# Performance work log

Hardware: AMD Instinct MI355X
Metric: run time of the kernel (lower is better)

## Reference

```python
import jax, jax.numpy as jnp
import numpy as np

N = 100000      # num nodes
E = 262144      # num directed edges (symmetrized)
DIN, H1, H2 = 58, 300, 100
EPS = 1e-15


def _glorot(k, shape):
    lim = float(np.sqrt(6.0 / (shape[0] + shape[1])))
    return jax.random.uniform(k, shape, jnp.float32, -lim, lim)


def setup_inputs() -> dict:
    key = jax.random.key(0)
    ks = jax.random.split(key, 16)
    x = jax.random.normal(ks[0], (N, DIN), jnp.float32)
    half = jax.random.randint(ks[1], (2, E // 2), 0, N, dtype=jnp.int32)
    edge_index = jnp.concatenate([half, half[::-1]], axis=1)  # symmetric graph
    neg_edge_index = jax.random.randint(ks[2], (2, E), 0, N, dtype=jnp.int32)
    return {
        "x": x,
        "edge_index": edge_index,
        "neg_edge_index": neg_edge_index,
        "conv1_w0": _glorot(ks[3], (DIN, H1)),
        "conv1_w1": _glorot(ks[4], (DIN, H1)),
        "conv1_b": jnp.zeros((H1,), jnp.float32),
        "conv2_w0": _glorot(ks[5], (H1, H2)),
        "conv2_w1": _glorot(ks[6], (H1, H2)),
        "conv2_b": jnp.zeros((H2,), jnp.float32),
        "conv3_w0": _glorot(ks[7], (H2, 1)),
        "conv3_w1": _glorot(ks[8], (H2, 1)),
        "conv3_b": jnp.zeros((1,), jnp.float32),
        "lin1_w": _glorot(ks[9], (DIN, H2)),
        "lin1_b": jnp.zeros((H2,), jnp.float32),
        "lin2_w": _glorot(ks[10], (DIN, H2)),
        "lin2_b": jnp.zeros((H2,), jnp.float32),
        "c1": jnp.array([0.5], jnp.float32),
        "c2": jnp.array([0.5], jnp.float32),
    }


def _cheb_norm(edge_index, n):
    # ChebConv K=2, sym normalization, lambda_max=2: edge weight = -d^-1/2 * d^-1/2
    row, col = edge_index[0], edge_index[1]
    deg = jax.ops.segment_sum(jnp.ones((edge_index.shape[1],), jnp.float32), row,
                              num_segments=n)
    dinv = jnp.where(deg > 0, jax.lax.rsqrt(jnp.maximum(deg, 1.0)), 0.0)
    return -dinv[row] * dinv[col]


def _cheb_conv(x, edge_index, w, w0, w1, b):
    # out = Tx0 @ W0 + Tx1 @ W1 + b, with Tx1 = -(D^-1/2 A D^-1/2) x
    src, dst = edge_index[0], edge_index[1]
    tx1 = jax.ops.segment_sum(w[:, None] * x[src], dst, num_segments=x.shape[0])
    return x @ w0 + tx1 @ w1 + b


def _link_logits(z, ei):
    return jnp.sum(z[ei[0]] * z[ei[1]], axis=1)


def reference(x, edge_index, neg_edge_index,
              conv1_w0, conv1_w1, conv1_b,
              conv2_w0, conv2_w1, conv2_b,
              conv3_w0, conv3_w1, conv3_b,
              lin1_w, lin1_b, lin2_w, lin2_b, c1, c2):
    n = x.shape[0]
    w = _cheb_norm(edge_index, n)  # eval mode: dropout_edge is identity
    x0 = x                          # eval mode: F.dropout is identity
    h = jax.nn.relu(_cheb_conv(x0, edge_index, w, conv1_w0, conv1_w1, conv1_b))
    x1 = jax.nn.relu(_cheb_conv(h, edge_index, w, conv2_w0, conv2_w1, conv2_b))
    xs = x1 + jax.nn.relu(x0 @ lin1_w + lin1_b)
    z = x1 + jax.nn.relu(x0 @ lin2_w + lin2_b)
    pos_loss = -jnp.mean(jnp.log(jax.nn.sigmoid(_link_logits(z, edge_index)) + EPS))
    neg_loss = -jnp.mean(jnp.log(1.0 - jax.nn.sigmoid(_link_logits(z, neg_edge_index)) + EPS))
    r_loss = pos_loss + neg_loss
    out = _cheb_conv(xs, edge_index, w, conv3_w0, conv3_w1, conv3_b).squeeze(-1)
    return (out, r_loss, c1, c2)
```

## Files before the change

### kernel.cpp

```cpp
#include <hip/hip_runtime.h>
#include <hip/hip_bf16.h>
#include <cstddef>

#define DIN 58
#define H1  300
#define H2  100

using bf16x8 = __attribute__((ext_vector_type(8))) short;
using bf16x4 = __attribute__((ext_vector_type(4))) short;
using f32x4  = __attribute__((ext_vector_type(4))) float;

__device__ inline unsigned short f2bf(float f) {
    union { float f; unsigned int u; } v; v.f = f;
    unsigned int r = v.u + 0x7fff + ((v.u >> 16) & 1);
    return (unsigned short)(r >> 16);
}
__device__ inline float bf2f(unsigned short h) {
    union { unsigned int u; float f; } v; v.u = ((unsigned int)h) << 16;
    return v.f;
}


__global__ void k_zero(float* __restrict__ p, long n) {
    long i = (long)blockIdx.x * 256 + threadIdx.x;
    long stride = (long)gridDim.x * 256;
    for (; i < n; i += stride) p[i] = 0.f;
}


__global__ void k_hist(const int* __restrict__ dst, int* __restrict__ cnt, int E) {
    int e = blockIdx.x * 256 + threadIdx.x;
    if (e < E) atomicAdd(&cnt[dst[e]], 1);
}

__global__ __launch_bounds__(256) void k_scan1(const int* __restrict__ cnt,
                                               int* __restrict__ offs,
                                               int* __restrict__ bsum, int N) {
    __shared__ int ts[256];
    int b = blockIdx.x, t = threadIdx.x;
    int base = b * 1024 + t * 4;
    int v0 = (base + 0 < N) ? cnt[base + 0] : 0;
    int v1 = (base + 1 < N) ? cnt[base + 1] : 0;
    int v2 = (base + 2 < N) ? cnt[base + 2] : 0;
    int v3 = (base + 3 < N) ? cnt[base + 3] : 0;
    ts[t] = v0 + v1 + v2 + v3;
    __syncthreads();
    for (int off = 1; off < 256; off <<= 1) {
        int u = (t >= off) ? ts[t - off] : 0;
        __syncthreads();
        ts[t] += u;
        __syncthreads();
    }
    int ex = (t > 0) ? ts[t - 1] : 0;
    if (base + 0 < N) offs[base + 0] = ex;
    if (base + 1 < N) offs[base + 1] = ex + v0;
    if (base + 2 < N) offs[base + 2] = ex + v0 + v1;
    if (base + 3 < N) offs[base + 3] = ex + v0 + v1 + v2;
    if (t == 255) bsum[b] = ts[255];
}

__global__ __launch_bounds__(256) void k_scan2(int* __restrict__ bsum, int nb) {
    __shared__ int ts[256];
    int t = threadIdx.x;
    ts[t] = (t < nb) ? bsum[t] : 0;
    __syncthreads();
    for (int off = 1; off < 256; off <<= 1) {
        int u = (t >= off) ? ts[t - off] : 0;
        __syncthreads();
        ts[t] += u;
        __syncthreads();
    }
    if (t < nb) bsum[t] = (t > 0) ? ts[t - 1] : 0;
}

__global__ void k_scan3(int* __restrict__ offs, const int* __restrict__ bsum,
                        int* __restrict__ cur, int N) {
    int i = blockIdx.x * 256 + threadIdx.x;
    if (i < N) {
        int v = offs[i] + bsum[i >> 10];
        offs[i] = v;
        cur[i] = v;
    }
}

__global__ void k_reorder2(const int* __restrict__ row, const int* __restrict__ col,
                           const int* __restrict__ cnt,
                           int* __restrict__ cur, int* __restrict__ srcS,
                           float* __restrict__ wS, int E) {
    int e = blockIdx.x * 256 + threadIdx.x;
    if (e < E) {
        int s = row[e], d = col[e];
        int p = atomicAdd(&cur[d], 1);
        float ds = (float)max(cnt[s], 1);
        float dd = (float)max(cnt[d], 1);
        srcS[p] = s;
        wS[p] = -rsqrtf(ds) * rsqrtf(dd);
    }
}


__global__ void k_cvtX(const float* __restrict__ x, unsigned short* __restrict__ Abf,
                       int N) {
    int t = blockIdx.x * 256 + threadIdx.x;
    int node = t >> 3, sub = t & 7;
    if (node >= N) return;
    bf16x8 o;
    #pragma unroll
    for (int j = 0; j < 8; ++j) {
        int c = sub * 8 + j;
        float v = (c < DIN) ? x[(size_t)node * DIN + c] : 0.f;
        o[j] = (short)f2bf(v);
    }
    *(bf16x8*)&Abf[(size_t)node * 128 + sub * 8] = o;
}


__global__ __launch_bounds__(256) void k_agg1b(const int* __restrict__ srcS,
                                               const float* __restrict__ wS,
                                               const int* __restrict__ offs,
                                               const int* __restrict__ cnt,
                                               unsigned short* __restrict__ Abf, int N) {
    int node = blockIdx.x * 32 + (threadIdx.x >> 3);
    int sub = threadIdx.x & 7;
    if (node >= N) return;
    int b0 = offs[node], b1 = b0 + cnt[node];
    float acc[8] = {};
    int i = b0;
    for (; i + 1 < b1; i += 2) {
        int s0 = srcS[i], s1 = srcS[i + 1];
        float w0 = wS[i], w1 = wS[i + 1];
        bf16x8 v0 = *(const bf16x8*)&Abf[(size_t)s0 * 128 + sub * 8];
        bf16x8 v1 = *(const bf16x8*)&Abf[(size_t)s1 * 128 + sub * 8];
        #pragma unroll
        for (int j = 0; j < 8; ++j)
            acc[j] += w0 * bf2f((unsigned short)v0[j]) + w1 * bf2f((unsigned short)v1[j]);
    }
    if (i < b1) {
        int s0 = srcS[i];
        float w0 = wS[i];
        bf16x8 v0 = *(const bf16x8*)&Abf[(size_t)s0 * 128 + sub * 8];
        #pragma unroll
        for (int j = 0; j < 8; ++j)
            acc[j] += w0 * bf2f((unsigned short)v0[j]);
    }
    bf16x8 o;
    #pragma unroll
    for (int j = 0; j < 8; ++j) o[j] = (short)f2bf(acc[j]);
    *(bf16x8*)&Abf[(size_t)node * 128 + 64 + sub * 8] = o;
}

__global__ __launch_bounds__(256) void k_agg2y(const unsigned short* __restrict__ hw1b,
                                               const int* __restrict__ srcS,
                                               const float* __restrict__ wS,
                                               const int* __restrict__ offs,
                                               const int* __restrict__ cnt,
                                               const float* __restrict__ c2b,
                                               const unsigned short* __restrict__ x1pb,
                                               unsigned short* __restrict__ rx1,
                                               unsigned short* __restrict__ rx2,
                                               const float* __restrict__ c3w0,
                                               const float* __restrict__ c3w1,
                                               const float* __restrict__ c3b,
                                               float* __restrict__ out,
                                               float* __restrict__ y1,
                                               int N) {
    int node = blockIdx.x * 16 + (threadIdx.x >> 4);
    int k = threadIdx.x & 15;
    bool live = node < N;
    float acc[8] = {};
    int b0 = 0, b1 = 0;
    if (live) { b0 = offs[node]; b1 = b0 + cnt[node]; }
    int i = b0;
    for (; i + 1 < b1; i += 2) {
        int s0 = srcS[i], s1 = srcS[i + 1];
        float w0 = wS[i], w1 = wS[i + 1];
        bf16x8 v0 = *(const bf16x8*)&hw1b[(size_t)s0 * 128 + k * 8];
        bf16x8 v1 = *(const bf16x8*)&hw1b[(size_t)s1 * 128 + k * 8];
        #pragma unroll
        for (int j = 0; j < 8; ++j)
            acc[j] += w0 * bf2f((unsigned short)v0[j]) + w1 * bf2f((unsigned short)v1[j]);
    }
    if (i < b1) {
        int s0 = srcS[i];
        float w0 = wS[i];
        bf16x8 v0 = *(const bf16x8*)&hw1b[(size_t)s0 * 128 + k * 8];
        #pragma unroll
        for (int j = 0; j < 8; ++j)
            acc[j] += w0 * bf2f((unsigned short)v0[j]);
    }

    float a0 = 0.f, a1 = 0.f;
    if (live) {
        size_t base = (size_t)node * 128 + k * 8;
        bf16x8 x1v = *(const bf16x8*)&x1pb[base];
        bf16x8 r1v = *(const bf16x8*)&rx1[base];
        bf16x8 r2v = *(const bf16x8*)&rx2[base];
        bf16x8 xo, zo;
        int f0 = k * 8;
        #pragma unroll
        for (int j = 0; j < 8; ++j) {
            int f = f0 + j;
            float bias = (f < H2) ? c2b[f] : 0.f;
            float v = fmaxf(bf2f((unsigned short)x1v[j]) + acc[j] + bias, 0.f);
            float xsf = v + bf2f((unsigned short)r1v[j]);
            float zf  = v + bf2f((unsigned short)r2v[j]);
            xo[j] = (short)f2bf(xsf);
            zo[j] = (short)f2bf(zf);
            if (f < H2) {
                a0 += xsf * c3w0[f];
                a1 += xsf * c3w1[f];
            }
        }
        *(bf16x8*)&rx1[base] = xo;
        *(bf16x8*)&rx2[base] = zo;
    }
    #pragma unroll
    for (int off = 8; off; off >>= 1) {
        a0 += __shfl_xor(a0, off);
        a1 += __shfl_xor(a1, off);
    }
    if (live && k == 0) {
        out[node] = a0 + c3b[0];
        y1[node]  = a1;
    }
}

__global__ void k_agg3(const float* __restrict__ y1, const int* __restrict__ srcS,
                       const float* __restrict__ wS, const int* __restrict__ offs,
                       const int* __restrict__ cnt, float* __restrict__ out, int N) {
    int node = blockIdx.x * 256 + threadIdx.x;
    if (node >= N) return;
    int b0 = offs[node], b1 = b0 + cnt[node];
    float a = 0.f;
    for (int i = b0; i < b1; ++i) a += wS[i] * y1[srcS[i]];
    out[node] += a;
}


__global__ void k_packB1X(const float* __restrict__ w0, const float* __restrict__ w1,
                          const float* __restrict__ lw1, const float* __restrict__ lw2,
                          unsigned short* __restrict__ Bt) {
    int i = blockIdx.x * 256 + threadIdx.x;
    if (i >= 640 * 128) return;
    int j = i >> 7, k = i & 127;
    float v = 0.f;
    if (j < H1) {
        if (k < DIN) v = w0[(size_t)k * H1 + j];
        else if (k >= 64 && k < 64 + DIN) v = w1[(size_t)(k - 64) * H1 + j];
    } else if (j >= 384 && j < 384 + H2) {
        if (k < DIN) v = lw1[(size_t)k * H2 + (j - 384)];
    } else if (j >= 512 && j < 512 + H2) {
        if (k < DIN) v = lw2[(size_t)k * H2 + (j - 512)];
    }
    Bt[i] = f2bf(v);
}

__global__ void k_packB2X(const float* __restrict__ w0, const float* __restrict__ w1,
                          unsigned short* __restrict__ Bt) {
    int i = blockIdx.x * 256 + threadIdx.x;
    if (i >= 256 * 320) return;
    int j = i / 320, k = i % 320;
    float v = 0.f;
    if (k < H1) {
        if (j < H2) v = w0[(size_t)k * H2 + j];
        else if (j >= 128 && j < 128 + H2) v = w1[(size_t)k * H2 + (j - 128)];
    }
    Bt[i] = f2bf(v);
}


__global__ __launch_bounds__(256) void gemm_c1(
    const unsigned short* __restrict__ A,
    const unsigned short* __restrict__ Bt,
    const float* __restrict__ c1b, const float* __restrict__ l1b,
    const float* __restrict__ l2b,
    unsigned short* __restrict__ hC,
    unsigned short* __restrict__ r1p,
    unsigned short* __restrict__ r2p,
    int M)
{
    __shared__ unsigned short As[128][40];
    __shared__ unsigned short Bs[128][40];
    const int tid = threadIdx.x;
    const int wave = tid >> 6, lane = tid & 63;
    const int wr = wave >> 1, wc = wave & 1;
    const int row0 = blockIdx.x * 128;
    const int col0 = blockIdx.y * 128;
    const int tr = tid >> 1;
    const int tk = (tid & 1) * 16;

    f32x4 acc[4][4] = {};

    for (int ks = 0; ks < 4; ++ks) {
        int kt = ks * 32;
        {
            int grow = row0 + tr;
            bf16x8 v0 = {}, v1 = {};
            if (grow < M) {
                const unsigned short* p = A + (size_t)grow * 128 + kt + tk;
                v0 = *(const bf16x8*)p;
                v1 = *(const bf16x8*)(p + 8);
            }
            *(bf16x8*)&As[tr][tk]     = v0;
            *(bf16x8*)&As[tr][tk + 8] = v1;
        }
        {
            int gcol = col0 + tr;
            const unsigned short* p = Bt + (size_t)gcol * 128 + kt + tk;
            *(bf16x8*)&Bs[tr][tk]     = *(const bf16x8*)p;
            *(bf16x8*)&Bs[tr][tk + 8] = *(const bf16x8*)(p + 8);
        }
        __syncthreads();

        const int kofs = (lane >> 4) * 8;
        bf16x8 af[4], bg[4];
        const int arow = wr * 64 + (lane & 15);
        const int bcol = wc * 64 + (lane & 15);
        #pragma unroll
        for (int m = 0; m < 4; ++m) af[m] = *(const bf16x8*)&As[arow + m * 16][kofs];
        #pragma unroll
        for (int n = 0; n < 4; ++n) bg[n] = *(const bf16x8*)&Bs[bcol + n * 16][kofs];
        #pragma unroll
        for (int m = 0; m < 4; ++m)
            #pragma unroll
            for (int n = 0; n < 4; ++n)
                acc[m][n] = __builtin_amdgcn_mfma_f32_16x16x32_bf16(bg[n], af[m], acc[m][n], 0, 0, 0);
        __syncthreads();
    }

    #pragma unroll
    for (int m = 0; m < 4; ++m) {
        int row = row0 + wr * 64 + m * 16 + (lane & 15);
        if (row >= M) continue;
        #pragma unroll
        for (int n = 0; n < 4; ++n) {
            int cbase = col0 + wc * 64 + n * 16 + (lane >> 4) * 4;
            bf16x4 o;
            if (cbase < 320) {
                #pragma unroll
                for (int i = 0; i < 4; ++i) {
                    int c = cbase + i;
                    float ov = (c < H1) ? fmaxf(acc[m][n][i] + c1b[c], 0.f) : 0.f;
                    o[i] = (short)f2bf(ov);
                }
                *(bf16x4*)&hC[(size_t)row * 320 + cbase] = o;
            } else if (cbase >= 384 && cbase < 512) {
                int c0 = cbase - 384;
                if (c0 < 128) {
                    #pragma unroll
                    for (int i = 0; i < 4; ++i) {
                        int c = c0 + i;
                        float ov = (c < H2) ? fmaxf(acc[m][n][i] + l1b[c], 0.f) : 0.f;
                        o[i] = (short)f2bf(ov);
                    }
                    *(bf16x4*)&r1p[(size_t)row * 128 + c0] = o;
                }
            } else if (cbase >= 512) {
                int c0 = cbase - 512;
                if (c0 < 128) {
                    #pragma unroll
                    for (int i = 0; i < 4; ++i) {
                        int c = c0 + i;
                        float ov = (c < H2) ? fmaxf(acc[m][n][i] + l2b[c], 0.f) : 0.f;
                        o[i] = (short)f2bf(ov);
                    }
                    *(bf16x4*)&r2p[(size_t)row * 128 + c0] = o;
                }
            }
        }
    }
}


__global__ __launch_bounds__(256) void gemm_c2(
    const unsigned short* __restrict__ A,
    const unsigned short* __restrict__ Bt,
    unsigned short* __restrict__ x1p,
    unsigned short* __restrict__ hwp,
    int M)
{
    __shared__ unsigned short As[128][40];
    __shared__ unsigned short Bs[128][40];
    const int tid = threadIdx.x;
    const int wave = tid >> 6, lane = tid & 63;
    const int wr = wave >> 1, wc = wave & 1;
    const int row0 = blockIdx.x * 128;
    const int col0 = blockIdx.y * 128;
    const int tr = tid >> 1;
    const int tk = (tid & 1) * 16;

    f32x4 acc[4][4] = {};

    for (int ks = 0; ks < 10; ++ks) {
        int kt = ks * 32;
        {
            int grow = row0 + tr;
            bf16x8 v0 = {}, v1 = {};
            if (grow < M) {
                const unsigned short* p = A + (size_t)grow * 320 + kt + tk;
                v0 = *(const bf16x8*)p;
                v1 = *(const bf16x8*)(p + 8);
            }
            *(bf16x8*)&As[tr][tk]     = v0;
            *(bf16x8*)&As[tr][tk + 8] = v1;
        }
        {
            int gcol = col0 + tr;
            const unsigned short* p = Bt + (size_t)gcol * 320 + kt + tk;
            *(bf16x8*)&Bs[tr][tk]     = *(const bf16x8*)p;
            *(bf16x8*)&Bs[tr][tk + 8] = *(const bf16x8*)(p + 8);
        }
        __syncthreads();

        const int kofs = (lane >> 4) * 8;
        bf16x8 af[4], bg[4];
        const int arow = wr * 64 + (lane & 15);
        const int bcol = wc * 64 + (lane & 15);
        #pragma unroll
        for (int m = 0; m < 4; ++m) af[m] = *(const bf16x8*)&As[arow + m * 16][kofs];
        #pragma unroll
        for (int n = 0; n < 4; ++n) bg[n] = *(const bf16x8*)&Bs[bcol + n * 16][kofs];
        #pragma unroll
        for (int m = 0; m < 4; ++m)
            #pragma unroll
            for (int n = 0; n < 4; ++n)
                acc[m][n] = __builtin_amdgcn_mfma_f32_16x16x32_bf16(bg[n], af[m], acc[m][n], 0, 0, 0);
        __syncthreads();
    }

    #pragma unroll
    for (int m = 0; m < 4; ++m) {
        int row = row0 + wr * 64 + m * 16 + (lane & 15);
        if (row >= M) continue;
        #pragma unroll
        for (int n = 0; n < 4; ++n) {
            int cbase = col0 + wc * 64 + n * 16 + (lane >> 4) * 4;
            bf16x4 o;
            if (cbase < 128) {
                #pragma unroll
                for (int i = 0; i < 4; ++i) {
                    int c = cbase + i;
                    o[i] = (short)((c < H2) ? f2bf(acc[m][n][i]) : (unsigned short)0);
                }
                *(bf16x4*)&x1p[(size_t)row * 128 + cbase] = o;
            } else {
                int c0 = cbase - 128;
                #pragma unroll
                for (int i = 0; i < 4; ++i) {
                    int c = c0 + i;
                    o[i] = (short)((c < H2) ? f2bf(acc[m][n][i]) : (unsigned short)0);
                }
                *(bf16x4*)&hwp[(size_t)row * 128 + c0] = o;
            }
        }
    }
}


__global__ __launch_bounds__(256) void k_loss2(const unsigned short* __restrict__ zb,
                                               const int* __restrict__ ei,
                                               const int* __restrict__ nei,
                                               int E, int En,
                                               float* __restrict__ part) {
    __shared__ float shP[4], shN[4];
    int k = threadIdx.x & 15;
    int grp = (blockIdx.x * 256 + threadIdx.x) >> 4;
    int ngrp = (gridDim.x * 256) >> 4;
    int tot = E + En;
    float sumP = 0.f, sumN = 0.f;

    for (int edge = grp; edge < tot; edge += ngrp) {
        int a, b;
        bool pos = edge < E;
        if (pos) { a = ei[edge]; b = ei[E + edge]; }
        else     { int e2 = edge - E; a = nei[e2]; b = nei[En + e2]; }
        bf16x8 va = *(const bf16x8*)&zb[(size_t)a * 128 + k * 8];
        bf16x8 vb = *(const bf16x8*)&zb[(size_t)b * 128 + k * 8];
        float d = 0.f;
        #pragma unroll
        for (int j = 0; j < 8; ++j)
            d += bf2f((unsigned short)va[j]) * bf2f((unsigned short)vb[j]);
        #pragma unroll
        for (int off = 8; off; off >>= 1) d += __shfl_xor(d, off);
        if (k == 0) {
            float s = 1.f / (1.f + expf(-d));
            if (pos) sumP += -logf(s + 1e-15f);
            else     sumN += -logf(1.f - s + 1e-15f);
        }
    }

    #pragma unroll
    for (int off = 32; off; off >>= 1) {
        sumP += __shfl_xor(sumP, off);
        sumN += __shfl_xor(sumN, off);
    }
    int wid = threadIdx.x >> 6;
    if ((threadIdx.x & 63) == 0) { shP[wid] = sumP; shN[wid] = sumN; }
    __syncthreads();
    if (threadIdx.x == 0)
        part[blockIdx.x * 2 + 0] = shP[0] + shP[1] + shP[2] + shP[3];
    if (threadIdx.x == 1)
        part[blockIdx.x * 2 + 1] = shN[0] + shN[1] + shN[2] + shN[3];
}

__global__ __launch_bounds__(256) void k_final2(const float* __restrict__ part, int nb,
                                                const float* __restrict__ c1,
                                                const float* __restrict__ c2,
                                                float* __restrict__ out, int N,
                                                float invEp, float invEn) {
    __shared__ float sp[4], sn[4];
    float aP = 0.f, aN = 0.f;
    for (int i = threadIdx.x; i < nb; i += 256) {
        aP += part[2 * i + 0];
        aN += part[2 * i + 1];
    }
    #pragma unroll
    for (int off = 32; off; off >>= 1) {
        aP += __shfl_xor(aP, off);
        aN += __shfl_xor(aN, off);
    }
    int wid = threadIdx.x >> 6;
    if ((threadIdx.x & 63) == 0) { sp[wid] = aP; sn[wid] = aN; }
    __syncthreads();
    if (threadIdx.x == 0) {
        float P = sp[0] + sp[1] + sp[2] + sp[3];
        float Nn = sn[0] + sn[1] + sn[2] + sn[3];
        out[N]     = P * invEp + Nn * invEn;
        out[N + 1] = c1[0];
        out[N + 2] = c2[0];
    }
}


extern "C" void kernel_launch(void* const* d_in, const int* in_sizes, int n_in,
                              void* d_out, int out_size, void* d_ws, size_t ws_size,
                              hipStream_t stream) {
    const float* x   = (const float*)d_in[0];
    const int*   ei  = (const int*)d_in[1];
    const int*   nei = (const int*)d_in[2];
    const float* c1w0 = (const float*)d_in[3];
    const float* c1w1 = (const float*)d_in[4];
    const float* c1b  = (const float*)d_in[5];
    const float* c2w0 = (const float*)d_in[6];
    const float* c2w1 = (const float*)d_in[7];
    const float* c2b  = (const float*)d_in[8];
    const float* c3w0 = (const float*)d_in[9];
    const float* c3w1 = (const float*)d_in[10];
    const float* c3b  = (const float*)d_in[11];
    const float* l1w  = (const float*)d_in[12];
    const float* l1b  = (const float*)d_in[13];
    const float* l2w  = (const float*)d_in[14];
    const float* l2b  = (const float*)d_in[15];
    const float* c1s  = (const float*)d_in[16];
    const float* c2s  = (const float*)d_in[17];

    const int N  = in_sizes[0] / DIN;
    const int E  = in_sizes[1] / 2;
    const int En = in_sizes[2] / 2;

    const int* row = ei;
    const int* col = ei + E;

    char* ws = (char*)d_ws;
    const size_t MB = 1024ull * 1024ull;
    const size_t KB = 1024ull;
    int*   srcS  = (int*)  (ws + 1 * MB);
    float* wS    = (float*)(ws + 2 * MB);
    int*   cnt   = (int*)  (ws + 3 * MB);
    int*   offs  = (int*)  (ws + 3 * MB + 512 * KB);
    int*   cur   = (int*)  (ws + 4 * MB);
    float* y1    = (float*)(ws + 5 * MB);
    int*   bsum  = (int*)  (ws + 5 * MB + 416 * KB);
    float* part  = (float*)(ws + 5 * MB + 420 * KB);
    unsigned short* Bt1X = (unsigned short*)(ws + 5 * MB + 448 * KB);
    unsigned short* Bt2  = (unsigned short*)(ws + 5 * MB + 640 * KB);
    unsigned short* Abf  = (unsigned short*)(ws + 6 * MB);
    unsigned short* r1b  = (unsigned short*)(ws + 31 * MB);
    unsigned short* r2b  = (unsigned short*)(ws + 56 * MB);
    unsigned short* x1pb = (unsigned short*)(ws + 81 * MB);
    unsigned short* hw1b = (unsigned short*)(ws + 106 * MB);
    unsigned short* hC   = (unsigned short*)(ws + 131 * MB);

    size_t hOff = 131 * MB;
    size_t avail = (ws_size > hOff + MB) ? (ws_size - hOff - MB) : 0;
    long maxRows = (long)(avail / 640);
    if (maxRows > N) maxRows = N;
    if (maxRows < 12500) maxRows = 12500;

    const int ZG = 1024;
    int gE = (E + 255) / 256;
    int gN = (N + 255) / 256;
    int NB = (N + 1023) / 1024;

    k_zero<<<ZG, 256, 0, stream>>>((float*)cnt, N);
    k_hist<<<gE, 256, 0, stream>>>(col, cnt, E);

    k_scan1<<<NB, 256, 0, stream>>>(cnt, offs, bsum, N);
    k_scan2<<<1, 256, 0, stream>>>(bsum, NB);
    k_scan3<<<gN, 256, 0, stream>>>(offs, bsum, cur, N);
    k_reorder2<<<gE, 256, 0, stream>>>(row, col, cnt, cur, srcS, wS, E);

    k_packB1X<<<(640 * 128 + 255) / 256, 256, 0, stream>>>(c1w0, c1w1, l1w, l2w, Bt1X);
    k_packB2X<<<(256 * 320 + 255) / 256, 256, 0, stream>>>(c2w0, c2w1, Bt2);

    k_cvtX<<<(N * 8 + 255) / 256, 256, 0, stream>>>(x, Abf, N);
    k_agg1b<<<(N + 31) / 32, 256, 0, stream>>>(srcS, wS, offs, cnt, Abf, N);

    for (long r0 = 0; r0 < N; r0 += maxRows) {
        long rc = (N - r0 < maxRows) ? (N - r0) : maxRows;
        dim3 g1((rc + 127) / 128, 5);
        gemm_c1<<<g1, 256, 0, stream>>>(Abf + (size_t)r0 * 128, Bt1X,
                                        c1b, l1b, l2b,
                                        hC, r1b + (size_t)r0 * 128, r2b + (size_t)r0 * 128,
                                        (int)rc);
        dim3 g2((rc + 127) / 128, 2);
        gemm_c2<<<g2, 256, 0, stream>>>(hC, Bt2,
                                        x1pb + (size_t)r0 * 128, hw1b + (size_t)r0 * 128,
                                        (int)rc);
    }

    k_agg2y<<<(N + 15) / 16, 256, 0, stream>>>(hw1b, srcS, wS, offs, cnt, c2b,
                                               x1pb, r1b, r2b,
                                               c3w0, c3w1, c3b, (float*)d_out, y1, N);

    k_agg3<<<gN, 256, 0, stream>>>(y1, srcS, wS, offs, cnt, (float*)d_out, N);

    const int LB = 2048;
    k_loss2<<<LB, 256, 0, stream>>>(r2b, ei, nei, E, En, part);
    k_final2<<<1, 256, 0, stream>>>(part, LB, c1s, c2s, (float*)d_out, N,
                                    1.0f / E, 1.0f / En);
}
```

Before: 329.4 us.

## Stage full-K A tiles in LDS and read B fragments directly from global

Both MFMA GEMMs now load the entire K extent of the A tile into shared memory at once: all of K=128 for gemm_c1, and two halves of 160 for gemm_c2. This replaces the per-32-K staging that needed two barriers per step. The B operand, which is small and heavily reused across blocks, is no longer staged in LDS; each lane reads its fragments straight from global memory and relies on caches. This cuts barrier count and LDS traffic, at the cost of more LDS per block (which may lower occupancy) and uncoalesced global B loads.

```diff
diff --git a/kernel.cpp b/kernel.cpp
--- a/kernel.cpp
+++ b/kernel.cpp
@@ -279,53 +279,44 @@
     unsigned short* __restrict__ r2p,
     int M)
 {
-    __shared__ unsigned short As[128][40];
-    __shared__ unsigned short Bs[128][40];
+    __shared__ unsigned short As[128][136];
     const int tid = threadIdx.x;
     const int wave = tid >> 6, lane = tid & 63;
     const int wr = wave >> 1, wc = wave & 1;
     const int row0 = blockIdx.x * 128;
     const int col0 = blockIdx.y * 128;
-    const int tr = tid >> 1;
-    const int tk = (tid & 1) * 16;
+
+    #pragma unroll
+    for (int q = 0; q < 8; ++q) {
+        int idx = tid + q * 256;
+        int r = idx >> 4;
+        int k8 = (idx & 15) * 8;
+        bf16x8 v = {};
+        int grow = row0 + r;
+        if (grow < M) v = *(const bf16x8*)(A + (size_t)grow * 128 + k8);
+        *(bf16x8*)&As[r][k8] = v;
+    }
+    __syncthreads();
 
     f32x4 acc[4][4] = {};
-
+    const int kofs = (lane >> 4) * 8;
+    const int arow = wr * 64 + (lane & 15);
+    const int bcol = col0 + wc * 64 + (lane & 15);
+
+    #pragma unroll
     for (int ks = 0; ks < 4; ++ks) {
-        int kt = ks * 32;
-        {
-            int grow = row0 + tr;
-            bf16x8 v0 = {}, v1 = {};
-            if (grow < M) {
-                const unsigned short* p = A + (size_t)grow * 128 + kt + tk;
-                v0 = *(const bf16x8*)p;
-                v1 = *(const bf16x8*)(p + 8);
-            }
-            *(bf16x8*)&As[tr][tk]     = v0;
-            *(bf16x8*)&As[tr][tk + 8] = v1;
-        }
-        {
-            int gcol = col0 + tr;
-            const unsigned short* p = Bt + (size_t)gcol * 128 + kt + tk;
-            *(bf16x8*)&Bs[tr][tk]     = *(const bf16x8*)p;
-            *(bf16x8*)&Bs[tr][tk + 8] = *(const bf16x8*)(p + 8);
-        }
-        __syncthreads();
-
-        const int kofs = (lane >> 4) * 8;
         bf16x8 af[4], bg[4];
-        const int arow = wr * 64 + (lane & 15);
-        const int bcol = wc * 64 + (lane & 15);
-        #pragma unroll
-        for (int m = 0; m < 4; ++m) af[m] = *(const bf16x8*)&As[arow + m * 16][kofs];
-        #pragma unroll
-        for (int n = 0; n < 4; ++n) bg[n] = *(const bf16x8*)&Bs[bcol + n * 16][kofs];
+        #pragma unroll
+        for (int n = 0; n < 4; ++n)
+            bg[n] = *(const bf16x8*)(Bt + (size_t)(bcol + n * 16) * 128 + ks * 32 + kofs);
+        #pragma unroll
+        for (int m = 0; m < 4; ++m)
+            af[m] = *(const bf16x8*)&As[arow + m * 16][ks * 32 + kofs];
         #pragma unroll
         for (int m = 0; m < 4; ++m)
             #pragma unroll
             for (int n = 0; n < 4; ++n)
                 acc[m][n] = __builtin_amdgcn_mfma_f32_16x16x32_bf16(bg[n], af[m], acc[m][n], 0, 0, 0);
-        __syncthreads();
     }
 
     #pragma unroll
@@ -379,52 +370,47 @@
     unsigned short* __restrict__ hwp,
     int M)
 {
-    __shared__ unsigned short As[128][40];
-    __shared__ unsigned short Bs[128][40];
+    __shared__ unsigned short As[128][168];
     const int tid = threadIdx.x;
     const int wave = tid >> 6, lane = tid & 63;
     const int wr = wave >> 1, wc = wave & 1;
     const int row0 = blockIdx.x * 128;
     const int col0 = blockIdx.y * 128;
-    const int tr = tid >> 1;
-    const int tk = (tid & 1) * 16;
 
     f32x4 acc[4][4] = {};
-
-    for (int ks = 0; ks < 10; ++ks) {
-        int kt = ks * 32;
-        {
-            int grow = row0 + tr;
-            bf16x8 v0 = {}, v1 = {};
-            if (grow < M) {
-                const unsigned short* p = A + (size_t)grow * 320 + kt + tk;
-                v0 = *(const bf16x8*)p;
-                v1 = *(const bf16x8*)(p + 8);
-            }
-            *(bf16x8*)&As[tr][tk]     = v0;
-            *(bf16x8*)&As[tr][tk + 8] = v1;
-        }
-        {
-            int gcol = col0 + tr;
-            const unsigned short* p = Bt + (size_t)gcol * 320 + kt + tk;
-            *(bf16x8*)&Bs[tr][tk]     = *(const bf16x8*)p;
-            *(bf16x8*)&Bs[tr][tk + 8] = *(const bf16x8*)(p + 8);
+    const int kofs = (lane >> 4) * 8;
+    const int arow = wr * 64 + (lane & 15);
+    const int bcol = col0 + wc * 64 + (lane & 15);
+
+    for (int ph = 0; ph < 2; ++ph) {
+        int kbase = ph * 160;
+        #pragma unroll
+        for (int q = 0; q < 10; ++q) {
+            int idx = tid + q * 256;
+            int r = idx / 20;
+            int k8 = (idx % 20) * 8;
+            bf16x8 v = {};
+            int grow = row0 + r;
+            if (grow < M) v = *(const bf16x8*)(A + (size_t)grow * 320 + kbase + k8);
+            *(bf16x8*)&As[r][k8] = v;
         }
         __syncthreads();
 
-        const int kofs = (lane >> 4) * 8;
-        bf16x8 af[4], bg[4];
-        const int arow = wr * 64 + (lane & 15);
-        const int bcol = wc * 64 + (lane & 15);
-        #pragma unroll
-        for (int m = 0; m < 4; ++m) af[m] = *(const bf16x8*)&As[arow + m * 16][kofs];
-        #pragma unroll
-        for (int n = 0; n < 4; ++n) bg[n] = *(const bf16x8*)&Bs[bcol + n * 16][kofs];
-        #pragma unroll
-        for (int m = 0; m < 4; ++m)
+        #pragma unroll
+        for (int ks = 0; ks < 5; ++ks) {
+            bf16x8 af[4], bg[4];
             #pragma unroll
             for (int n = 0; n < 4; ++n)
-                acc[m][n] = __builtin_amdgcn_mfma_f32_16x16x32_bf16(bg[n], af[m], acc[m][n], 0, 0, 0);
+                bg[n] = *(const bf16x8*)(Bt + (size_t)(bcol + n * 16) * 320 + kbase + ks * 32 + kofs);
+            #pragma unroll
+            for (int m = 0; m < 4; ++m)
+                af[m] = *(const bf16x8*)&As[arow + m * 16][ks * 32 + kofs];
+            #pragma unroll
+            for (int m = 0; m < 4; ++m)
+                #pragma unroll
+                for (int n = 0; n < 4; ++n)
+                    acc[m][n] = __builtin_amdgcn_mfma_f32_16x16x32_bf16(bg[n], af[m], acc[m][n], 0, 0, 0);
+        }
         __syncthreads();
     }
 
```

Result: slower. 370.3 us (+12.4%).
